# Performance work log

Measured on AMD Instinct MI355X. Metric: run time of the kernel, lower is better.

Reference implementation:

```python
import jax, jax.numpy as jnp
from jax import lax
import numpy as np

ND1, ND2 = 48, 8   # stage_configs
LAMB = 1.5
EPS = 1e-12


def _make_proj(scale, n_views):
    H, W = 512 // scale, 640 // scale
    f = 700.0 / scale
    K = np.array([[f, 0, W / 2], [0, f, H / 2], [0, 0, 1]], np.float32)
    mats = []
    for v in range(n_views):
        a = 0.04 * v
        R = np.array([[np.cos(a), 0, np.sin(a)], [0, 1, 0], [-np.sin(a), 0, np.cos(a)]], np.float32)
        E = np.eye(4, dtype=np.float32)
        E[:3, :3] = R
        E[0, 3] = 20.0 * v
        Kin = np.eye(4, dtype=np.float32)
        Kin[:3, :3] = K
        mats.append(np.stack([E, Kin]))
    return jnp.asarray(np.stack(mats))[None]  # [1,V,2,4,4]


def setup_inputs():
    key = jax.random.key(0)
    ks = jax.random.split(key, 5)
    return {
        'feats1': jax.random.normal(ks[0], (1, 3, 32, 128, 160), jnp.float32),
        'feats2': jax.random.normal(ks[1], (1, 3, 16, 256, 320), jnp.float32),
        'proj1': _make_proj(4, 3),
        'proj2': _make_proj(2, 3),
        'depth_values': jnp.linspace(425.0, 935.0, ND1, dtype=jnp.float32)[None],
        'img': jax.random.normal(ks[2], (1, 3, 512, 640), jnp.float32),
        'w1': jax.random.normal(ks[3], (1, 32, 3, 3, 3), jnp.float32) * 0.05,
        'b1': jnp.zeros((1,), jnp.float32),
        'w2': jax.random.normal(ks[4], (1, 16, 3, 3, 3), jnp.float32) * 0.05,
        'b2': jnp.zeros((1,), jnp.float32),
    }


def _compose(p):
    # p: [B,2,4,4] -> K @ E[:3,:4] placed in top 3 rows of the extrinsic
    top = jnp.einsum('bij,bjk->bik', p[:, 1, :3, :3], p[:, 0, :3, :4])
    return p[:, 0].at[:, :3, :4].set(top)


def _bilinear(fea, x, y):
    # grid_sample(mode='bilinear', padding_mode='zeros', align_corners=False)
    # fea [B,C,H,W]; x,y pixel coords [B,P] -> [B,C,P]
    B, C, H, W = fea.shape
    flat = fea.reshape(B, C, H * W)
    x0, y0 = jnp.floor(x), jnp.floor(y)

    def gather(xi, yi):
        valid = (xi >= 0) & (xi <= W - 1) & (yi >= 0) & (yi <= H - 1)
        idx = (jnp.clip(yi, 0, H - 1) * W + jnp.clip(xi, 0, W - 1)).astype(jnp.int32)
        v = jnp.take_along_axis(flat, idx[:, None, :], axis=2)
        return jnp.where(valid[:, None, :], v, 0.0)

    wx, wy = x - x0, y - y0
    return (gather(x0, y0) * ((1 - wx) * (1 - wy))[:, None]
            + gather(x0 + 1, y0) * (wx * (1 - wy))[:, None]
            + gather(x0, y0 + 1) * ((1 - wx) * wy)[:, None]
            + gather(x0 + 1, y0 + 1) * (wx * wy)[:, None])


def _homo_warp(src_fea, src_proj, ref_proj, depth_samps):
    B, C, H, W = src_fea.shape
    D = depth_samps.shape[1]
    proj = jnp.einsum('bij,bjk->bik', src_proj, jnp.linalg.inv(ref_proj))
    rot, trans = proj[:, :3, :3], proj[:, :3, 3:4]
    yy, xx = jnp.meshgrid(jnp.arange(H, dtype=src_fea.dtype),
                          jnp.arange(W, dtype=src_fea.dtype), indexing='ij')
    xyz = jnp.stack([xx.ravel(), yy.ravel(), jnp.ones(H * W, src_fea.dtype)])  # [3,HW]
    rot_xyz = jnp.einsum('bij,jp->bip', rot, xyz)                               # [B,3,HW]
    pxyz = rot_xyz[:, :, None, :] * depth_samps.reshape(B, 1, D, -1) + trans[:, :, None, :]  # [B,3,D,HW]
    gx = pxyz[:, 0] / pxyz[:, 2] / ((W - 1) / 2) - 1.0
    gy = pxyz[:, 1] / pxyz[:, 2] / ((H - 1) / 2) - 1.0
    ix = ((gx + 1.0) * W - 1.0) / 2.0  # unnormalize, align_corners=False
    iy = ((gy + 1.0) * H - 1.0) / 2.0
    warped = _bilinear(src_fea, ix.reshape(B, -1), iy.reshape(B, -1))
    return warped.reshape(B, C, D, H, W)


def _conv3d(x, w, b):
    y = lax.conv_general_dilated(x, w, (1, 1, 1), 'SAME',
                                 dimension_numbers=('NCDHW', 'OIDHW', 'NCDHW'))
    return y + b.reshape(1, -1, 1, 1, 1)


def _stage(feats, projs, depth_samps, w, b):
    # feats [B,V,C,H,W], projs [B,V,2,4,4], depth_samps [B,D,H,W]
    B, V, C, H, W = feats.shape
    D = depth_samps.shape[1]
    ref_proj = _compose(projs[:, 0])
    ref_vol = jnp.broadcast_to(feats[:, 0][:, :, None], (B, C, D, H, W))
    vsum, vsq = ref_vol, ref_vol ** 2
    for v in range(1, V):  # small fixed number of views
        wv = _homo_warp(feats[:, v], _compose(projs[:, v]), ref_proj, depth_samps)
        vsum = vsum + wv
        vsq = vsq + wv ** 2
    variance = vsq / V - (vsum / V) ** 2
    prob = jax.nn.softmax(_conv3d(variance, w, b)[:, 0], axis=1)  # [B,D,H,W]
    depth = jnp.sum(prob * depth_samps, axis=1)                   # [B,H,W]
    p = jnp.pad(prob, ((0, 0), (1, 2), (0, 0), (0, 0)))
    sum4 = p[:, 0:D] + p[:, 1:D + 1] + p[:, 2:D + 2] + p[:, 3:D + 3]  # 4*avg_pool3d((4,1,1))
    di = jnp.sum(prob * jnp.arange(D, dtype=prob.dtype)[None, :, None, None], axis=1)
    di = jnp.clip(di.astype(jnp.int32), 0, D - 1)
    conf = jnp.take_along_axis(sum4, di[:, None], axis=1)[:, 0]
    exp_var = LAMB * jnp.sqrt(jnp.sum((depth_samps - depth[:, None]) ** 2 * prob, axis=1))
    return depth, conf, exp_var


def _forward(feats1, feats2, proj1, proj2, depth_values, img, w1, b1, w2, b2):
    B, _, Hi, Wi = img.shape
    H1, W1 = Hi // 4, Wi // 4
    H2, W2 = Hi // 2, Wi // 2
    # stage 1: depth_values is [B,D] -> uniform sampling path
    dmin, dmax = depth_values[:, 0], depth_values[:, -1]
    step1 = (dmax - dmin) / (ND1 - 1)
    s1 = dmin[:, None] + jnp.arange(ND1, dtype=jnp.float32)[None] * step1[:, None]
    samps1 = jnp.broadcast_to(s1[:, :, None, None], (B, ND1, H1, W1))
    d1, c1, v1 = _stage(feats1, proj1, samps1, w1, b1)
    # stage 2: detach + bilinear upsample + uncertainty-aware samples
    cur_d = jax.image.resize(lax.stop_gradient(d1)[:, None], (B, 1, H2, W2), 'bilinear')
    cur_v = jax.image.resize(lax.stop_gradient(v1)[:, None], (B, 1, H2, W2), 'bilinear')
    low = -jnp.minimum(cur_d, cur_v)
    step2 = (cur_v - low) / (ND2 - 1.0)
    samps2 = cur_d + low + step2 * jnp.arange(ND2, dtype=jnp.float32)[None, :, None, None] + EPS
    d2, c2, v2 = _stage(feats2, proj2, samps2, w2, b2)
    return (d1, c1, v1, d2, c2, v2)


def reference(feats1, feats2, proj1, proj2, depth_values, img, w1, b1, w2, b2):
    return _forward(feats1, feats2, proj1, proj2, depth_values, img, w1, b1, w2, b2)
```

## Files before the change

kernel.cpp:

```cpp
#include <hip/hip_runtime.h>
#include <math.h>


typedef _Float16 half2_t __attribute__((ext_vector_type(2)));
typedef _Float16 half8_t __attribute__((ext_vector_type(8)));

union U4H { uint4 u; half2_t h[4]; };
union U2H { uint2 u; half2_t h[2]; };

static __device__ inline float fdot2f(half2_t a, half2_t b, float c) {
#if __has_builtin(__builtin_amdgcn_fdot2)
  return __builtin_amdgcn_fdot2(a, b, c, false);
#else
  return c + (float)a[0] * (float)b[0] + (float)a[1] * (float)b[1];
#endif
}

__global__ void setup_mats_kernel(const float* __restrict__ proj1,
                                  const float* __restrict__ proj2,
                                  const float* __restrict__ depthv, int nd,
                                  float* __restrict__ ws,
                                  const float* __restrict__ w1,
                                  const float* __restrict__ w2,
                                  _Float16* __restrict__ w2a,
                                  _Float16* __restrict__ w2b) {
  const int tid = threadIdx.x;
  if (w2a != nullptr) {
    for (int i = tid; i < 27 * 32; i += 256) {
      int c = i % 32, r = i / 32, kd = r % 3, t = r / 3;
      w2a[(t * 3 + kd) * 32 + c] = (_Float16)w1[c * 27 + kd * 9 + t];
    }
    for (int i = tid; i < 27 * 16; i += 256) {
      int c = i % 16, r = i / 16, kd = r % 3, t = r / 3;
      w2b[(t * 3 + kd) * 16 + c] = (_Float16)w2[c * 27 + kd * 9 + t];
    }
  }
  if (tid != 0) return;
  for (int s = 0; s < 2; ++s) {
    const float* P = s ? proj2 : proj1;
    double comp[3][4][4];
    for (int v = 0; v < 3; ++v) {
      const float* E = P + v * 32;
      const float* K = P + v * 32 + 16;
      for (int r = 0; r < 3; ++r)
        for (int c = 0; c < 4; ++c) {
          double acc = 0.0;
          for (int k = 0; k < 3; ++k) acc += (double)K[r * 4 + k] * (double)E[k * 4 + c];
          comp[v][r][c] = acc;
        }
      for (int c = 0; c < 4; ++c) comp[v][3][c] = (double)E[12 + c];
    }
    double a[4][8];
    for (int r = 0; r < 4; ++r)
      for (int c = 0; c < 4; ++c) {
        a[r][c] = comp[0][r][c];
        a[r][4 + c] = (r == c) ? 1.0 : 0.0;
      }
    for (int col = 0; col < 4; ++col) {
      int piv = col;
      double best = fabs(a[col][col]);
      for (int r = col + 1; r < 4; ++r) {
        double t = fabs(a[r][col]);
        if (t > best) { best = t; piv = r; }
      }
      if (piv != col)
        for (int c = 0; c < 8; ++c) { double t = a[col][c]; a[col][c] = a[piv][c]; a[piv][c] = t; }
      double dv = a[col][col];
      for (int c = 0; c < 8; ++c) a[col][c] /= dv;
      for (int r = 0; r < 4; ++r)
        if (r != col) {
          double f = a[r][col];
          if (f != 0.0)
            for (int c = 0; c < 8; ++c) a[r][c] -= f * a[col][c];
        }
    }
    for (int v = 1; v < 3; ++v) {
      double Pm[3][4];
      for (int r = 0; r < 3; ++r)
        for (int c = 0; c < 4; ++c) {
          double acc = 0.0;
          for (int k = 0; k < 4; ++k) acc += comp[v][r][k] * a[k][4 + c];
          Pm[r][c] = acc;
        }
      float* o = ws + s * 24 + (v - 1) * 12;
      o[0] = (float)Pm[0][0]; o[1] = (float)Pm[0][1]; o[2] = (float)Pm[0][2];
      o[3] = (float)Pm[1][0]; o[4] = (float)Pm[1][1]; o[5] = (float)Pm[1][2];
      o[6] = (float)Pm[2][0]; o[7] = (float)Pm[2][1]; o[8] = (float)Pm[2][2];
      o[9] = (float)Pm[0][3]; o[10] = (float)Pm[1][3]; o[11] = (float)Pm[2][3];
    }
  }
  ws[48] = depthv[0];
  ws[49] = (depthv[nd - 1] - depthv[0]) / 47.0f;
}

template <int C, int H, int W>
__global__ void transpose_f16_kernel(const float* __restrict__ in,
                                     _Float16* __restrict__ out) {
  __shared__ float s_t[C][33];
  const int v = blockIdx.z, h = blockIdx.y, w0 = blockIdx.x * 32;
  const int tid = threadIdx.x;
  for (int r = tid; r < C * 32; r += 256) {
    int c = r >> 5, w = r & 31;
    s_t[c][w] = in[((size_t)(v * C + c) * H + h) * W + w0 + w];
  }
  __syncthreads();
  for (int r = tid; r < 32 * C; r += 256) {
    int w = r / C, c = r - (r / C) * C;
    out[((size_t)(v * H + h) * W + w0 + w) * C + c] = (_Float16)s_t[c][w];
  }
}

template <int D, int H, int W>
__device__ inline void stage2_range(const float* __restrict__ prev_d,
                                    const float* __restrict__ prev_v,
                                    int gy, int gx, float& base, float& st) {
  constexpr int SH = H / 2, SW = W / 2;
  float syf = 0.5f * (float)gy - 0.25f;
  float sxf = 0.5f * (float)gx - 0.25f;
  syf = fminf(fmaxf(syf, 0.0f), (float)(SH - 1));
  sxf = fminf(fmaxf(sxf, 0.0f), (float)(SW - 1));
  int sy0 = (int)syf, sx0 = (int)sxf;
  float fy2 = syf - (float)sy0, fx2 = sxf - (float)sx0;
  int sy1 = min(sy0 + 1, SH - 1), sx1 = min(sx0 + 1, SW - 1);
  int j00 = sy0 * SW + sx0, j01 = sy0 * SW + sx1;
  int j10 = sy1 * SW + sx0, j11 = sy1 * SW + sx1;
  float cd = (prev_d[j00] * (1.f - fx2) + prev_d[j01] * fx2) * (1.f - fy2) +
             (prev_d[j10] * (1.f - fx2) + prev_d[j11] * fx2) * fy2;
  float cv = (prev_v[j00] * (1.f - fx2) + prev_v[j01] * fx2) * (1.f - fy2) +
             (prev_v[j10] * (1.f - fx2) + prev_v[j11] * fx2) * fy2;
  float lo = -fminf(cd, cv);
  base = cd + lo + 1e-12f;
  st = (cv - lo) / (float)(D - 1);
}

template <int D, int H, int W>
__global__ void range_kernel(const float* __restrict__ prev_d,
                             const float* __restrict__ prev_v,
                             float2* __restrict__ rng) {
  int pix = blockIdx.x * 256 + threadIdx.x;
  if (pix >= H * W) return;
  float b, s;
  stage2_range<D, H, W>(prev_d, prev_v, pix / W, pix % W, b, s);
  rng[pix] = make_float2(b, s);
}

template <int C, int DTOT, int H, int W, bool STAGE2>
__launch_bounds__(256)
__global__ void gather_var_kernel(const _Float16* __restrict__ feats,
                                  const float* __restrict__ mats,
                                  const float* __restrict__ dpar,
                                  const float2* __restrict__ rng,
                                  _Float16* __restrict__ var_out) {
  constexpr int C8 = C / 8;
  const int idx = blockIdx.x * 256 + threadIdx.x;
  if (idx >= DTOT * H * W * C8) return;
  const int cg = idx % C8;
  const int t = idx / C8;
  const int gx = t % W;
  const int t2 = t / W;
  const int gy = t2 % H;
  const int d = t2 / H;
  const int pix = gy * W + gx;

  float base, st;
  if constexpr (STAGE2) {
    float2 r = rng[pix];
    base = r.x;
    st = r.y;
  } else {
    base = dpar[0];
    st = dpar[1];
  }
  const float dep = base + (float)d * st;

  const half8_t* fp = (const half8_t*)feats;
  half8_t rh = fp[(size_t)pix * C8 + cg];
  float s[8], q[8];
#pragma unroll
  for (int j = 0; j < 8; ++j) {
    float x = (float)rh[j];
    s[j] = x;
    q[j] = x * x;
  }

#pragma unroll
  for (int v = 0; v < 2; ++v) {
    const float* M = mats + v * 12;
    float fx = (float)gx, fy = (float)gy;
    float X = (M[0] * fx + M[1] * fy + M[2]) * dep + M[9];
    float Y = (M[3] * fx + M[4] * fy + M[5]) * dep + M[10];
    float Z = (M[6] * fx + M[7] * fy + M[8]) * dep + M[11];
    float inv = 1.0f / Z;
    float xz = X * inv, yz = Y * inv;
    float gxn = xz * (2.0f / (float)(W - 1)) - 1.0f;
    float gyn = yz * (2.0f / (float)(H - 1)) - 1.0f;
    float ix = ((gxn + 1.0f) * (float)W - 1.0f) * 0.5f;
    float iy = ((gyn + 1.0f) * (float)H - 1.0f) * 0.5f;
    float x0f = floorf(ix), y0f = floorf(iy);
    float wx = ix - x0f, wy = iy - y0f;
    float x1f = x0f + 1.0f, y1f = y0f + 1.0f;
    bool vx0 = (x0f >= 0.0f) && (x0f <= (float)(W - 1));
    bool vx1 = (x1f >= 0.0f) && (x1f <= (float)(W - 1));
    bool vy0 = (y0f >= 0.0f) && (y0f <= (float)(H - 1));
    bool vy1 = (y1f >= 0.0f) && (y1f <= (float)(H - 1));
    int xc0 = (int)fminf(fmaxf(x0f, 0.0f), (float)(W - 1));
    int xc1 = (int)fminf(fmaxf(x1f, 0.0f), (float)(W - 1));
    int yc0 = (int)fminf(fmaxf(y0f, 0.0f), (float)(H - 1));
    int yc1 = (int)fminf(fmaxf(y1f, 0.0f), (float)(H - 1));
    float wxm = 1.0f - wx, wym = 1.0f - wy;
    float a00 = (vx0 && vy0) ? wxm * wym : 0.0f;
    float a10 = (vx1 && vy0) ? wx * wym : 0.0f;
    float a01 = (vx0 && vy1) ? wxm * wy : 0.0f;
    float a11 = (vx1 && vy1) ? wx * wy : 0.0f;
    const size_t vb = (size_t)(v + 1) * H * W * C8 + cg;
    half8_t p00 = fp[vb + (size_t)(yc0 * W + xc0) * C8];
    half8_t p10 = fp[vb + (size_t)(yc0 * W + xc1) * C8];
    half8_t p01 = fp[vb + (size_t)(yc1 * W + xc0) * C8];
    half8_t p11 = fp[vb + (size_t)(yc1 * W + xc1) * C8];
#pragma unroll
    for (int j = 0; j < 8; ++j) {
      float g = a00 * (float)p00[j] + a10 * (float)p10[j] +
                a01 * (float)p01[j] + a11 * (float)p11[j];
      s[j] += g;
      q[j] += g * g;
    }
  }
  half8_t o;
#pragma unroll
  for (int j = 0; j < 8; ++j) {
    float m = s[j] * (1.0f / 3.0f);
    o[j] = (_Float16)(q[j] * (1.0f / 3.0f) - m * m);
  }
  *(half8_t*)(var_out + ((size_t)(d * C8 + cg) * (H * W) + pix) * 8) = o;
}

template <int C, int DTOT, int DC, int H, int W>
__launch_bounds__(256)
__global__ void conv_cost_kernel(const uint4* __restrict__ var_in,
                                 const _Float16* __restrict__ w2h,
                                 const float* __restrict__ bconv,
                                 float* __restrict__ g_cost) {
  constexpr int TH = 8, TW = 8, WB = 10, HALO = 100, NPX = 64;
  constexpr int NS = DC + 2;
  constexpr int CPG = C / 4;
  constexpr int HW = H * W;
  constexpr int C8 = C / 8;
  constexpr int REC = (CPG == 8) ? 16 : 8;

  __shared__ __align__(16) unsigned char s_wv_raw[4 * NS * HALO * REC];
  __shared__ __align__(16) unsigned char s_wt_raw[4 * 27 * REC];
  __shared__ float s_part[4 * DC * NPX];

  uint4* s_wv4 = (uint4*)s_wv_raw;
  uint2* s_wv2 = (uint2*)s_wv_raw;
  uint4* s_wt4 = (uint4*)s_wt_raw;
  uint2* s_wt2 = (uint2*)s_wt_raw;

  const int tid = threadIdx.x;
  const int lane = tid & 63;
  const int grp = tid >> 6;
  const int h0 = blockIdx.y * TH;
  const int w0 = blockIdx.x * TW;
  const int d0 = blockIdx.z * DC;

  if (lane < 27) {
    if constexpr (CPG == 8)
      s_wt4[grp * 27 + lane] = *(const uint4*)(w2h + lane * C + grp * CPG);
    else
      s_wt2[grp * 27 + lane] = *(const uint2*)(w2h + lane * C + grp * CPG);
  }

  int gidx[2], ldi[2];
  bool act[2], gval[2];
#pragma unroll
  for (int k = 0; k < 2; ++k) {
    int i = lane + k * 64;
    act[k] = (i < HALO);
    int hy = i / WB, hx = i - (i / WB) * WB;
    int gy = h0 + hy - 1, gx = w0 + hx - 1;
    gval[k] = act[k] && gy >= 0 && gy < H && gx >= 0 && gx < W;
    gidx[k] = gval[k] ? (gy * W + gx) : 0;
    ldi[k] = i;
  }

  if constexpr (CPG == 8) {
    uint4 pf[NS][2];
#pragma unroll
    for (int s = 0; s < NS; ++s) {
      int ds = d0 - 1 + s;
      bool dv = (ds >= 0) && (ds < DTOT);
#pragma unroll
      for (int k = 0; k < 2; ++k) {
        uint4 r = make_uint4(0u, 0u, 0u, 0u);
        if (dv && gval[k]) r = var_in[(size_t)(ds * C8 + grp) * HW + gidx[k]];
        pf[s][k] = r;
      }
    }
#pragma unroll
    for (int s = 0; s < NS; ++s)
#pragma unroll
      for (int k = 0; k < 2; ++k)
        if (act[k]) s_wv4[(grp * NS + s) * HALO + ldi[k]] = pf[s][k];
  } else {
    uint2 pf[NS][2];
#pragma unroll
    for (int s = 0; s < NS; ++s) {
      int ds = d0 - 1 + s;
      bool dv = (ds >= 0) && (ds < DTOT);
#pragma unroll
      for (int k = 0; k < 2; ++k) {
        uint2 r = make_uint2(0u, 0u);
        if (dv && gval[k])
          r = ((const uint2*)var_in)[((size_t)(ds * C8 + (grp >> 1)) * HW + gidx[k]) * 2 +
                                     (grp & 1)];
        pf[s][k] = r;
      }
    }
#pragma unroll
    for (int s = 0; s < NS; ++s)
#pragma unroll
      for (int k = 0; k < 2; ++k)
        if (act[k]) s_wv2[(grp * NS + s) * HALO + ldi[k]] = pf[s][k];
  }

  const int opx = lane;
  const int py = opx >> 3, pxx = opx & 7;

  float accA[NS], accB[NS], accC[NS];
#pragma unroll
  for (int s = 0; s < NS; ++s) { accA[s] = 0.f; accB[s] = 0.f; accC[s] = 0.f; }

#pragma unroll
  for (int t = 0; t < 9; ++t) {
    const int kh = t / 3, kw = t - 3 * kh;
    const int hp = (py + kh) * WB + (pxx + kw);
    if constexpr (CPG == 8) {
      U4H w0v, w1v, w2v;
      w0v.u = s_wt4[grp * 27 + t * 3 + 0];
      w1v.u = s_wt4[grp * 27 + t * 3 + 1];
      w2v.u = s_wt4[grp * 27 + t * 3 + 2];
#pragma unroll
      for (int s = 0; s < NS; ++s) {
        U4H v;
        v.u = s_wv4[(grp * NS + s) * HALO + hp];
        float a = 0.f, b = 0.f, c = 0.f;
#pragma unroll
        for (int j = 0; j < 4; ++j) {
          a = fdot2f(v.h[j], w0v.h[j], a);
          b = fdot2f(v.h[j], w1v.h[j], b);
          c = fdot2f(v.h[j], w2v.h[j], c);
        }
        accA[s] += a;
        accB[s] += b;
        accC[s] += c;
      }
    } else {
      U2H w0v, w1v, w2v;
      w0v.u = s_wt2[grp * 27 + t * 3 + 0];
      w1v.u = s_wt2[grp * 27 + t * 3 + 1];
      w2v.u = s_wt2[grp * 27 + t * 3 + 2];
#pragma unroll
      for (int s = 0; s < NS; ++s) {
        U2H v;
        v.u = s_wv2[(grp * NS + s) * HALO + hp];
        float a = 0.f, b = 0.f, c = 0.f;
#pragma unroll
        for (int j = 0; j < 2; ++j) {
          a = fdot2f(v.h[j], w0v.h[j], a);
          b = fdot2f(v.h[j], w1v.h[j], b);
          c = fdot2f(v.h[j], w2v.h[j], c);
        }
        accA[s] += a;
        accB[s] += b;
        accC[s] += c;
      }
    }
  }

#pragma unroll
  for (int j = 0; j < DC; ++j)
    s_part[grp * (DC * NPX) + j * NPX + opx] = accA[j] + accB[j + 1] + accC[j + 2];
  __syncthreads();

  const float bias = bconv[0];
  for (int i = tid; i < DC * NPX; i += 256) {
    float v = bias + s_part[i] + s_part[DC * NPX + i] + s_part[2 * DC * NPX + i] +
              s_part[3 * DC * NPX + i];
    int dd = i / NPX, o = i - dd * NPX;
    int oy = o / TW, ox = o - oy * TW;
    g_cost[(size_t)(d0 + dd) * (H * W) + (h0 + oy) * W + (w0 + ox)] = v;
  }
}

template <int D, int H, int W, bool STAGE2>
__global__ void epilogue_kernel(const float* __restrict__ g_cost,
                                const float* __restrict__ dpar,
                                const float2* __restrict__ rng,
                                float* __restrict__ out_d,
                                float* __restrict__ out_c,
                                float* __restrict__ out_v) {
  int pix = blockIdx.x * 256 + threadIdx.x;
  if (pix >= H * W) return;
  float base, st;
  if constexpr (STAGE2) {
    float2 r = rng[pix];
    base = r.x;
    st = r.y;
  } else {
    base = dpar[0];
    st = dpar[1];
  }
  float c[D];
#pragma unroll
  for (int dd = 0; dd < D; ++dd) c[dd] = g_cost[(size_t)dd * (H * W) + pix];
  float mx = -3.0e38f;
#pragma unroll
  for (int dd = 0; dd < D; ++dd) mx = fmaxf(mx, c[dd]);
  float se = 0.f;
#pragma unroll
  for (int dd = 0; dd < D; ++dd) {
    float e = expf(c[dd] - mx);
    c[dd] = e;
    se += e;
  }
  float depth = 0.f, dif = 0.f;
#pragma unroll
  for (int dd = 0; dd < D; ++dd) {
    float p = c[dd] / se;
    c[dd] = p;
    depth += p * (base + (float)dd * st);
    dif += p * (float)dd;
  }
  int di = (int)dif;
  di = min(max(di, 0), D - 1);
  float conf = 0.f;
#pragma unroll
  for (int dd = 0; dd < D; ++dd)
    if (dd >= di - 1 && dd <= di + 2) conf += c[dd];
  float ev = 0.f;
#pragma unroll
  for (int dd = 0; dd < D; ++dd) {
    float sv = base + (float)dd * st - depth;
    ev += sv * sv * c[dd];
  }
  ev = 1.5f * sqrtf(ev);
  out_d[pix] = depth;
  out_c[pix] = conf;
  out_v[pix] = ev;
}


template <int C, int DTOT, int DC, int TH, int TW, int H, int W, bool STAGE2, bool EPI>
__launch_bounds__(256)
__global__ void cost_kernel(const float* __restrict__ feats,
                            const float* __restrict__ wconv,
                            const float* __restrict__ bconv,
                            const float* __restrict__ mats,
                            const float* __restrict__ dpar,
                            const float* __restrict__ prev_d,
                            const float* __restrict__ prev_v,
                            float* __restrict__ g_cost,
                            float* __restrict__ out_d,
                            float* __restrict__ out_c,
                            float* __restrict__ out_v) {
  constexpr int HB = TH + 2, WB = TW + 2, HALO = HB * WB, NPX = TH * TW;
  constexpr int HP = HALO + 1;
  constexpr int CG = C / 4;
  constexpr int NS = DC + 2;
  constexpr int VITEMS = HALO * C;

  __shared__ float s_var[2][C * HP];
  __shared__ float s_cost[DC * NPX];
  __shared__ float s_w[C * 27];
  __shared__ float s_rx[2][HALO], s_ry[2][HALO], s_rz[2][HALO];
  __shared__ float s_cw[2][2][4][HALO];
  __shared__ int s_ci[2][2][4][HALO];
  __shared__ int s_gidx[HALO];
  __shared__ float s_dbase[HALO], s_dstep[HALO];
  __shared__ unsigned char s_inb[HALO];

  const int tid = threadIdx.x;
  const int h0 = blockIdx.y * TH;
  const int w0 = blockIdx.x * TW;
  const int d0 = EPI ? 0 : blockIdx.z * DC;

  for (int i = tid; i < C * 27; i += 256) s_w[i] = wconv[i];

  for (int i = tid; i < HALO; i += 256) {
    int hy = i / WB, hx = i - hy * WB;
    int gy = h0 + hy - 1, gx = w0 + hx - 1;
    bool inb = (gy >= 0) && (gy < H) && (gx >= 0) && (gx < W);
    s_inb[i] = inb ? 1 : 0;
    s_gidx[i] = inb ? (gy * W + gx) : 0;
    float fx = (float)gx, fy = (float)gy;
#pragma unroll
    for (int v = 0; v < 2; ++v) {
      const float* M = mats + v * 12;
      s_rx[v][i] = M[0] * fx + M[1] * fy + M[2];
      s_ry[v][i] = M[3] * fx + M[4] * fy + M[5];
      s_rz[v][i] = M[6] * fx + M[7] * fy + M[8];
    }
    if constexpr (STAGE2) {
      float b, stp;
      stage2_range<DTOT, H, W>(prev_d, prev_v, gy, gx, b, stp);
      s_dbase[i] = b;
      s_dstep[i] = stp;
    } else {
      s_dbase[i] = dpar[0];
      s_dstep[i] = dpar[1];
    }
  }
  {
    float bias = bconv[0];
    for (int i = tid; i < DC * NPX; i += 256) s_cost[i] = bias;
  }
  __syncthreads();

  auto do_coords = [&](int ds, int b, int i) {
    int v = (i >= HALO) ? 1 : 0;
    int px = i - v * HALO;
    float dep = s_dbase[px] + (float)ds * s_dstep[px];
    const float* M = mats + v * 12;
    float X = s_rx[v][px] * dep + M[9];
    float Y = s_ry[v][px] * dep + M[10];
    float Z = s_rz[v][px] * dep + M[11];
    float inv = 1.0f / Z;
    float xz = X * inv, yz = Y * inv;
    float gxn = xz * (2.0f / (float)(W - 1)) - 1.0f;
    float gyn = yz * (2.0f / (float)(H - 1)) - 1.0f;
    float ix = ((gxn + 1.0f) * (float)W - 1.0f) * 0.5f;
    float iy = ((gyn + 1.0f) * (float)H - 1.0f) * 0.5f;
    float x0f = floorf(ix), y0f = floorf(iy);
    float wx = ix - x0f, wy = iy - y0f;
    float x1f = x0f + 1.0f, y1f = y0f + 1.0f;
    bool vx0 = (x0f >= 0.0f) && (x0f <= (float)(W - 1));
    bool vx1 = (x1f >= 0.0f) && (x1f <= (float)(W - 1));
    bool vy0 = (y0f >= 0.0f) && (y0f <= (float)(H - 1));
    bool vy1 = (y1f >= 0.0f) && (y1f <= (float)(H - 1));
    int xc0 = (int)fminf(fmaxf(x0f, 0.0f), (float)(W - 1));
    int xc1 = (int)fminf(fmaxf(x1f, 0.0f), (float)(W - 1));
    int yc0 = (int)fminf(fmaxf(y0f, 0.0f), (float)(H - 1));
    int yc1 = (int)fminf(fmaxf(y1f, 0.0f), (float)(H - 1));
    s_ci[b][v][0][px] = yc0 * W + xc0;
    s_ci[b][v][1][px] = yc0 * W + xc1;
    s_ci[b][v][2][px] = yc1 * W + xc0;
    s_ci[b][v][3][px] = yc1 * W + xc1;
    float wxm = 1.0f - wx, wym = 1.0f - wy;
    s_cw[b][v][0][px] = (vx0 && vy0) ? wxm * wym : 0.0f;
    s_cw[b][v][1][px] = (vx1 && vy0) ? wx * wym : 0.0f;
    s_cw[b][v][2][px] = (vx0 && vy1) ? wxm * wy : 0.0f;
    s_cw[b][v][3][px] = (vx1 && vy1) ? wx * wy : 0.0f;
  };

  auto do_variance = [&](int b, int b2, int i) {
    int c = i / HALO, px = i - (i / HALO) * HALO;
    float var = 0.f;
    if (s_inb[px]) {
      const float* f0 = feats + (size_t)c * (H * W);
      float rr = f0[s_gidx[px]];
      float sum = rr, ssq = rr * rr;
#pragma unroll
      for (int v = 0; v < 2; ++v) {
        const float* fv = feats + ((size_t)(v + 1) * C + c) * (H * W);
        float val = s_cw[b][v][0][px] * fv[s_ci[b][v][0][px]] +
                    s_cw[b][v][1][px] * fv[s_ci[b][v][1][px]] +
                    s_cw[b][v][2][px] * fv[s_ci[b][v][2][px]] +
                    s_cw[b][v][3][px] * fv[s_ci[b][v][3][px]];
        sum += val;
        ssq += val * val;
      }
      float m = sum / 3.0f;
      var = ssq / 3.0f - m * m;
    }
    s_var[b2][c * HP + px] = var;
  };

  auto conv_accum = [&](int ds, int sb) {
    for (int i = tid; i < NPX * 4; i += 256) {
      int grp = i / NPX, opx = i - grp * NPX;
      int py = opx / TW, pxx = opx - py * TW;
      float a0 = 0.f, a1 = 0.f, a2 = 0.f;
      int cbase = grp * CG;
#pragma unroll
      for (int kh = 0; kh < 3; ++kh) {
#pragma unroll
        for (int kw = 0; kw < 3; ++kw) {
          int hp = (py + kh) * WB + (pxx + kw);
#pragma unroll
          for (int cc = 0; cc < CG; ++cc) {
            int c = cbase + cc;
            float vv = s_var[sb][c * HP + hp];
            const float* wp = s_w + c * 27 + kh * 3 + kw;
            a0 += vv * wp[0];
            a1 += vv * wp[9];
            a2 += vv * wp[18];
          }
        }
      }
      int t0 = ds + 1 - d0;
      int t1 = ds - d0;
      int t2 = ds - 1 - d0;
      if (t0 >= 0 && t0 < DC) atomicAdd(&s_cost[t0 * NPX + opx], a0);
      if (t1 >= 0 && t1 < DC) atomicAdd(&s_cost[t1 * NPX + opx], a1);
      if (t2 >= 0 && t2 < DC) atomicAdd(&s_cost[t2 * NPX + opx], a2);
    }
  };

  {
    int ds0 = d0 - 1;
    if (ds0 >= 0 && ds0 < DTOT)
      for (int i = tid; i < 2 * HALO; i += 256) do_coords(ds0, 0, i);
  }
  __syncthreads();

  for (int s = 0; s <= NS; ++s) {
    const int ds = d0 - 1 + s;
    const bool val_cur = (s < NS) && (ds >= 0) && (ds < DTOT);
    const bool val_next = (s + 1 < NS) && (ds + 1 >= 0) && (ds + 1 < DTOT);
    const bool val_prev = (s >= 1) && (ds - 1 >= 0) && (ds - 1 < DTOT);
    if (val_cur)
      for (int i = tid; i < VITEMS; i += 256) do_variance(s & 1, s & 1, i);
    if (val_next)
      for (int i = tid; i < 2 * HALO; i += 256) do_coords(ds + 1, (s + 1) & 1, i);
    if (val_prev) conv_accum(ds - 1, (s - 1) & 1);
    __syncthreads();
  }

  if constexpr (!EPI) {
    for (int i = tid; i < DC * NPX; i += 256) {
      int dd = i / NPX, opx = i - dd * NPX;
      int py = opx / TW, pxx = opx - py * TW;
      g_cost[(size_t)(d0 + dd) * (H * W) + (h0 + py) * W + (w0 + pxx)] = s_cost[i];
    }
  } else if (tid < NPX) {
    const int opx = tid;
    const int py = opx / TW, pxx = opx - py * TW;
    const int hp = (py + 1) * WB + (pxx + 1);
    const float base = s_dbase[hp], st = s_dstep[hp];
    float mx = -3.0e38f;
    for (int dd = 0; dd < DTOT; ++dd) mx = fmaxf(mx, s_cost[dd * NPX + opx]);
    float se = 0.f;
    for (int dd = 0; dd < DTOT; ++dd) {
      float e = expf(s_cost[dd * NPX + opx] - mx);
      s_cost[dd * NPX + opx] = e;
      se += e;
    }
    float depth = 0.f, dif = 0.f;
    for (int dd = 0; dd < DTOT; ++dd) {
      float p = s_cost[dd * NPX + opx] / se;
      s_cost[dd * NPX + opx] = p;
      depth += p * (base + (float)dd * st);
      dif += p * (float)dd;
    }
    int di = (int)dif;
    di = min(max(di, 0), DTOT - 1);
    float conf = 0.f;
    for (int k = di - 1; k <= di + 2; ++k)
      if (k >= 0 && k < DTOT) conf += s_cost[k * NPX + opx];
    float ev = 0.f;
    for (int dd = 0; dd < DTOT; ++dd) {
      float sv = base + (float)dd * st - depth;
      ev += sv * sv * s_cost[dd * NPX + opx];
    }
    ev = 1.5f * sqrtf(ev);
    int gy = h0 + py, gx = w0 + pxx;
    out_d[gy * W + gx] = depth;
    out_c[gy * W + gx] = conf;
    out_v[gy * W + gx] = ev;
  }
}

extern "C" void kernel_launch(void* const* d_in, const int* in_sizes, int n_in,
                              void* d_out, int out_size, void* d_ws, size_t ws_size,
                              hipStream_t stream) {
  const float* feats1 = (const float*)d_in[0];
  const float* feats2 = (const float*)d_in[1];
  const float* proj1 = (const float*)d_in[2];
  const float* proj2 = (const float*)d_in[3];
  const float* depthv = (const float*)d_in[4];
  const float* w1 = (const float*)d_in[6];
  const float* b1 = (const float*)d_in[7];
  const float* w2 = (const float*)d_in[8];
  const float* b2 = (const float*)d_in[9];
  float* out = (float*)d_out;
  float* ws = (float*)d_ws;

  const int nd = in_sizes[4];
  const size_t F1 = (size_t)3 * 32 * 128 * 160;
  const size_t F2 = (size_t)3 * 16 * 256 * 320;
  const size_t COST1 = (size_t)48 * 128 * 160;
  const size_t COST2 = (size_t)8 * 256 * 320;
  const size_t VAR1 = (size_t)48 * 128 * 160 * 32;
  const size_t VAR2 = (size_t)8 * 256 * 320 * 16;
  const size_t RNG2 = (size_t)2 * 256 * 320;
  const size_t HDR = 1408;
  const size_t HUGE_FLOATS =
      HDR + COST1 + COST2 + F1 / 2 + F2 / 2 + VAR1 / 2 + VAR2 / 2 + RNG2;
  const bool huge = ws_size >= HUGE_FLOATS * sizeof(float);
  const bool mid = ws_size >= (64 + COST1) * sizeof(float);

  float* d1 = out;
  float* c1 = out + 20480;
  float* v1 = out + 40960;
  float* d2 = out + 61440;
  float* c2 = out + 143360;
  float* v2 = out + 225280;

  dim3 g1c(160 / 8, 128 / 8, 8), g1f(160 / 8, 128 / 8, 1), g2(320 / 8, 256 / 8, 1);

  if (huge) {
    _Float16* w2a = (_Float16*)(ws + 64);
    _Float16* w2b = (_Float16*)(ws + 512);
    float* cost1 = ws + HDR;
    float* cost2 = cost1 + COST1;
    _Float16* f1t = (_Float16*)(cost2 + COST2);
    _Float16* f2t = (_Float16*)(cost2 + COST2 + F1 / 2);
    _Float16* var1 = (_Float16*)(cost2 + COST2 + F1 / 2 + F2 / 2);
    _Float16* var2 = (_Float16*)(cost2 + COST2 + F1 / 2 + F2 / 2 + VAR1 / 2);
    float2* rng2 = (float2*)(cost2 + COST2 + F1 / 2 + F2 / 2 + VAR1 / 2 + VAR2 / 2);
    setup_mats_kernel<<<1, 256, 0, stream>>>(proj1, proj2, depthv, nd, ws, w1, w2, w2a, w2b);
    transpose_f16_kernel<32, 128, 160><<<dim3(5, 128, 3), 256, 0, stream>>>(feats1, f1t);
    transpose_f16_kernel<16, 256, 320><<<dim3(10, 256, 3), 256, 0, stream>>>(feats2, f2t);
    gather_var_kernel<32, 48, 128, 160, false>
        <<<(int)((VAR1 / 8 + 255) / 256), 256, 0, stream>>>(f1t, ws, ws + 48, nullptr, var1);
    conv_cost_kernel<32, 48, 6, 128, 160><<<g1c, 256, 0, stream>>>(
        (const uint4*)var1, w2a, b1, cost1);
    epilogue_kernel<48, 128, 160, false><<<80, 256, 0, stream>>>(
        cost1, ws + 48, nullptr, d1, c1, v1);
    range_kernel<8, 256, 320><<<320, 256, 0, stream>>>(d1, v1, rng2);
    gather_var_kernel<16, 8, 256, 320, true>
        <<<(int)((VAR2 / 8 + 255) / 256), 256, 0, stream>>>(f2t, ws + 24, ws + 48, rng2, var2);
    conv_cost_kernel<16, 8, 8, 256, 320><<<dim3(40, 32, 1), 256, 0, stream>>>(
        (const uint4*)var2, w2b, b2, cost2);
    epilogue_kernel<8, 256, 320, true><<<320, 256, 0, stream>>>(
        cost2, ws + 48, rng2, d2, c2, v2);
  } else if (mid) {
    float* cost1 = ws + 64;
    setup_mats_kernel<<<1, 256, 0, stream>>>(proj1, proj2, depthv, nd, ws, w1, w2,
                                             nullptr, nullptr);
    cost_kernel<32, 48, 8, 8, 8, 128, 160, false, false><<<dim3(20, 16, 6), 256, 0, stream>>>(
        feats1, w1, b1, ws, ws + 48, nullptr, nullptr, cost1, nullptr, nullptr, nullptr);
    epilogue_kernel<48, 128, 160, false><<<80, 256, 0, stream>>>(
        cost1, ws + 48, nullptr, d1, c1, v1);
    cost_kernel<16, 8, 8, 8, 8, 256, 320, true, true><<<g2, 256, 0, stream>>>(
        feats2, w2, b2, ws + 24, ws + 48, d1, v1, nullptr, d2, c2, v2);
  } else {
    setup_mats_kernel<<<1, 256, 0, stream>>>(proj1, proj2, depthv, nd, ws, w1, w2,
                                             nullptr, nullptr);
    cost_kernel<32, 48, 48, 8, 8, 128, 160, false, true><<<g1f, 256, 0, stream>>>(
        feats1, w1, b1, ws, ws + 48, nullptr, nullptr, nullptr, d1, c1, v1);
    cost_kernel<16, 8, 8, 8, 8, 256, 320, true, true><<<g2, 256, 0, stream>>>(
        feats2, w2, b2, ws + 24, ws + 48, d1, v1, nullptr, d2, c2, v2);
  }
}
```

Measured before the change: 223.7 us.

## Fuse transposes, per-pixel gather over all channels, fuse stage-2 epilogue into conv

After: 224.7 us. Within noise of the previous version (+0.5%).

```diff
diff --git a/kernel.cpp b/kernel.cpp
--- a/kernel.cpp
+++ b/kernel.cpp
@@ -94,19 +94,35 @@
 }
 
 template <int C, int H, int W>
-__global__ void transpose_f16_kernel(const float* __restrict__ in,
-                                     _Float16* __restrict__ out) {
-  __shared__ float s_t[C][33];
-  const int v = blockIdx.z, h = blockIdx.y, w0 = blockIdx.x * 32;
+__device__ inline void transpose_body(const float* __restrict__ in,
+                                      _Float16* __restrict__ out,
+                                      int x, int h, int v, float* s_t) {
   const int tid = threadIdx.x;
+  const int w0 = x * 32;
   for (int r = tid; r < C * 32; r += 256) {
     int c = r >> 5, w = r & 31;
-    s_t[c][w] = in[((size_t)(v * C + c) * H + h) * W + w0 + w];
+    s_t[c * 33 + w] = in[((size_t)(v * C + c) * H + h) * W + w0 + w];
   }
   __syncthreads();
   for (int r = tid; r < 32 * C; r += 256) {
     int w = r / C, c = r - (r / C) * C;
-    out[((size_t)(v * H + h) * W + w0 + w) * C + c] = (_Float16)s_t[c][w];
+    out[((size_t)(v * H + h) * W + w0 + w) * C + c] = (_Float16)s_t[c * 33 + w];
+  }
+}
+
+__global__ void transpose_both_kernel(const float* __restrict__ in1,
+                                      _Float16* __restrict__ out1,
+                                      const float* __restrict__ in2,
+                                      _Float16* __restrict__ out2) {
+  __shared__ float s_t[32 * 33];
+  int bid = blockIdx.x;
+  if (bid < 1920) {
+    int x = bid % 5, h = (bid / 5) % 128, v = bid / (5 * 128);
+    transpose_body<32, 128, 160>(in1, out1, x, h, v, s_t);
+  } else {
+    int b = bid - 1920;
+    int x = b % 10, h = (b / 10) % 256, v = b / (10 * 256);
+    transpose_body<16, 256, 320>(in2, out2, x, h, v, s_t);
   }
 }
 
@@ -153,11 +169,9 @@
                                   _Float16* __restrict__ var_out) {
   constexpr int C8 = C / 8;
   const int idx = blockIdx.x * 256 + threadIdx.x;
-  if (idx >= DTOT * H * W * C8) return;
-  const int cg = idx % C8;
-  const int t = idx / C8;
-  const int gx = t % W;
-  const int t2 = t / W;
+  if (idx >= DTOT * H * W) return;
+  const int gx = idx % W;
+  const int t2 = idx / W;
   const int gy = t2 % H;
   const int d = t2 / H;
   const int pix = gy * W + gx;
@@ -174,13 +188,16 @@
   const float dep = base + (float)d * st;
 
   const half8_t* fp = (const half8_t*)feats;
-  half8_t rh = fp[(size_t)pix * C8 + cg];
-  float s[8], q[8];
-#pragma unroll
-  for (int j = 0; j < 8; ++j) {
-    float x = (float)rh[j];
-    s[j] = x;
-    q[j] = x * x;
+  float s[C], q[C];
+#pragma unroll
+  for (int cg = 0; cg < C8; ++cg) {
+    half8_t r = fp[(size_t)pix * C8 + cg];
+#pragma unroll
+    for (int j = 0; j < 8; ++j) {
+      float x = (float)r[j];
+      s[cg * 8 + j] = x;
+      q[cg * 8 + j] = x * x;
+    }
   }
 
 #pragma unroll
@@ -212,34 +229,48 @@
     float a10 = (vx1 && vy0) ? wx * wym : 0.0f;
     float a01 = (vx0 && vy1) ? wxm * wy : 0.0f;
     float a11 = (vx1 && vy1) ? wx * wy : 0.0f;
-    const size_t vb = (size_t)(v + 1) * H * W * C8 + cg;
-    half8_t p00 = fp[vb + (size_t)(yc0 * W + xc0) * C8];
-    half8_t p10 = fp[vb + (size_t)(yc0 * W + xc1) * C8];
-    half8_t p01 = fp[vb + (size_t)(yc1 * W + xc0) * C8];
-    half8_t p11 = fp[vb + (size_t)(yc1 * W + xc1) * C8];
+    const size_t vb = (size_t)(v + 1) * H * W * C8;
+    const size_t i00 = vb + (size_t)(yc0 * W + xc0) * C8;
+    const size_t i10 = vb + (size_t)(yc0 * W + xc1) * C8;
+    const size_t i01 = vb + (size_t)(yc1 * W + xc0) * C8;
+    const size_t i11 = vb + (size_t)(yc1 * W + xc1) * C8;
+#pragma unroll
+    for (int cg = 0; cg < C8; ++cg) {
+      half8_t p00 = fp[i00 + cg];
+      half8_t p10 = fp[i10 + cg];
+      half8_t p01 = fp[i01 + cg];
+      half8_t p11 = fp[i11 + cg];
+#pragma unroll
+      for (int j = 0; j < 8; ++j) {
+        float g = a00 * (float)p00[j] + a10 * (float)p10[j] +
+                  a01 * (float)p01[j] + a11 * (float)p11[j];
+        s[cg * 8 + j] += g;
+        q[cg * 8 + j] += g * g;
+      }
+    }
+  }
+#pragma unroll
+  for (int cg = 0; cg < C8; ++cg) {
+    half8_t o;
 #pragma unroll
     for (int j = 0; j < 8; ++j) {
-      float g = a00 * (float)p00[j] + a10 * (float)p10[j] +
-                a01 * (float)p01[j] + a11 * (float)p11[j];
-      s[j] += g;
-      q[j] += g * g;
-    }
-  }
-  half8_t o;
-#pragma unroll
-  for (int j = 0; j < 8; ++j) {
-    float m = s[j] * (1.0f / 3.0f);
-    o[j] = (_Float16)(q[j] * (1.0f / 3.0f) - m * m);
-  }
-  *(half8_t*)(var_out + ((size_t)(d * C8 + cg) * (H * W) + pix) * 8) = o;
-}
-
-template <int C, int DTOT, int DC, int H, int W>
+      float m = s[cg * 8 + j] * (1.0f / 3.0f);
+      o[j] = (_Float16)(q[cg * 8 + j] * (1.0f / 3.0f) - m * m);
+    }
+    *(half8_t*)(var_out + ((size_t)(d * C8 + cg) * (H * W) + pix) * 8) = o;
+  }
+}
+
+template <int C, int DTOT, int DC, int H, int W, bool EPI>
 __launch_bounds__(256)
 __global__ void conv_cost_kernel(const uint4* __restrict__ var_in,
                                  const _Float16* __restrict__ w2h,
                                  const float* __restrict__ bconv,
-                                 float* __restrict__ g_cost) {
+                                 float* __restrict__ g_cost,
+                                 const float2* __restrict__ rng,
+                                 float* __restrict__ out_d,
+                                 float* __restrict__ out_c,
+                                 float* __restrict__ out_v) {
   constexpr int TH = 8, TW = 8, WB = 10, HALO = 100, NPX = 64;
   constexpr int NS = DC + 2;
   constexpr int CPG = C / 4;
@@ -383,12 +414,62 @@
   __syncthreads();
 
   const float bias = bconv[0];
-  for (int i = tid; i < DC * NPX; i += 256) {
-    float v = bias + s_part[i] + s_part[DC * NPX + i] + s_part[2 * DC * NPX + i] +
-              s_part[3 * DC * NPX + i];
-    int dd = i / NPX, o = i - dd * NPX;
-    int oy = o / TW, ox = o - oy * TW;
-    g_cost[(size_t)(d0 + dd) * (H * W) + (h0 + oy) * W + (w0 + ox)] = v;
+  if constexpr (!EPI) {
+    for (int i = tid; i < DC * NPX; i += 256) {
+      float v = bias + s_part[i] + s_part[DC * NPX + i] + s_part[2 * DC * NPX + i] +
+                s_part[3 * DC * NPX + i];
+      int dd = i / NPX, o = i - dd * NPX;
+      int oy = o / TW, ox = o - oy * TW;
+      g_cost[(size_t)(d0 + dd) * (H * W) + (h0 + oy) * W + (w0 + ox)] = v;
+    }
+  } else {
+    for (int i = tid; i < DC * NPX; i += 256)
+      s_part[i] = bias + s_part[i] + s_part[DC * NPX + i] + s_part[2 * DC * NPX + i] +
+                  s_part[3 * DC * NPX + i];
+    __syncthreads();
+    if (tid < NPX) {
+      const int gy = h0 + py, gx = w0 + pxx;
+      const int pix = gy * W + gx;
+      float2 r = rng[pix];
+      const float base = r.x, stp = r.y;
+      float c[DC];
+#pragma unroll
+      for (int dd = 0; dd < DC; ++dd) c[dd] = s_part[dd * NPX + opx];
+      float mx = -3.0e38f;
+#pragma unroll
+      for (int dd = 0; dd < DC; ++dd) mx = fmaxf(mx, c[dd]);
+      float se = 0.f;
+#pragma unroll
+      for (int dd = 0; dd < DC; ++dd) {
+        float e = expf(c[dd] - mx);
+        c[dd] = e;
+        se += e;
+      }
+      float depth = 0.f, dif = 0.f;
+#pragma unroll
+      for (int dd = 0; dd < DC; ++dd) {
+        float p = c[dd] / se;
+        c[dd] = p;
+        depth += p * (base + (float)dd * stp);
+        dif += p * (float)dd;
+      }
+      int di = (int)dif;
+      di = min(max(di, 0), DC - 1);
+      float conf = 0.f;
+#pragma unroll
+      for (int dd = 0; dd < DC; ++dd)
+        if (dd >= di - 1 && dd <= di + 2) conf += c[dd];
+      float ev = 0.f;
+#pragma unroll
+      for (int dd = 0; dd < DC; ++dd) {
+        float sv = base + (float)dd * stp - depth;
+        ev += sv * sv * c[dd];
+      }
+      ev = 1.5f * sqrtf(ev);
+      out_d[pix] = depth;
+      out_c[pix] = conf;
+      out_v[pix] = ev;
+    }
   }
 }
 
@@ -706,7 +787,7 @@
   float* c2 = out + 143360;
   float* v2 = out + 225280;
 
-  dim3 g1c(160 / 8, 128 / 8, 8), g1f(160 / 8, 128 / 8, 1), g2(320 / 8, 256 / 8, 1);
+  dim3 g1f(160 / 8, 128 / 8, 1), g2(320 / 8, 256 / 8, 1);
 
   if (huge) {
     _Float16* w2a = (_Float16*)(ws + 64);
@@ -719,21 +800,20 @@
     _Float16* var2 = (_Float16*)(cost2 + COST2 + F1 / 2 + F2 / 2 + VAR1 / 2);
     float2* rng2 = (float2*)(cost2 + COST2 + F1 / 2 + F2 / 2 + VAR1 / 2 + VAR2 / 2);
     setup_mats_kernel<<<1, 256, 0, stream>>>(proj1, proj2, depthv, nd, ws, w1, w2, w2a, w2b);
-    transpose_f16_kernel<32, 128, 160><<<dim3(5, 128, 3), 256, 0, stream>>>(feats1, f1t);
-    transpose_f16_kernel<16, 256, 320><<<dim3(10, 256, 3), 256, 0, stream>>>(feats2, f2t);
+    transpose_both_kernel<<<1920 + 7680, 256, 0, stream>>>(feats1, f1t, feats2, f2t);
     gather_var_kernel<32, 48, 128, 160, false>
-        <<<(int)((VAR1 / 8 + 255) / 256), 256, 0, stream>>>(f1t, ws, ws + 48, nullptr, var1);
-    conv_cost_kernel<32, 48, 6, 128, 160><<<g1c, 256, 0, stream>>>(
-        (const uint4*)var1, w2a, b1, cost1);
+        <<<(int)((48 * 128 * 160 + 255) / 256), 256, 0, stream>>>(f1t, ws, ws + 48, nullptr,
+                                                                  var1);
+    conv_cost_kernel<32, 48, 4, 128, 160, false><<<dim3(20, 16, 12), 256, 0, stream>>>(
+        (const uint4*)var1, w2a, b1, cost1, nullptr, nullptr, nullptr, nullptr);
     epilogue_kernel<48, 128, 160, false><<<80, 256, 0, stream>>>(
         cost1, ws + 48, nullptr, d1, c1, v1);
     range_kernel<8, 256, 320><<<320, 256, 0, stream>>>(d1, v1, rng2);
     gather_var_kernel<16, 8, 256, 320, true>
-        <<<(int)((VAR2 / 8 + 255) / 256), 256, 0, stream>>>(f2t, ws + 24, ws + 48, rng2, var2);
-    conv_cost_kernel<16, 8, 8, 256, 320><<<dim3(40, 32, 1), 256, 0, stream>>>(
-        (const uint4*)var2, w2b, b2, cost2);
-    epilogue_kernel<8, 256, 320, true><<<320, 256, 0, stream>>>(
-        cost2, ws + 48, rng2, d2, c2, v2);
+        <<<(int)((8 * 256 * 320 + 255) / 256), 256, 0, stream>>>(f2t, ws + 24, ws + 48, rng2,
+                                                                 var2);
+    conv_cost_kernel<16, 8, 8, 256, 320, true><<<dim3(40, 32, 1), 256, 0, stream>>>(
+        (const uint4*)var2, w2b, b2, nullptr, rng2, d2, c2, v2);
   } else if (mid) {
     float* cost1 = ws + 64;
     setup_mats_kernel<<<1, 256, 0, stream>>>(proj1, proj2, depthv, nd, ws, w1, w2,
```
